# Performance work log

Hardware: AMD Instinct MI355X
Metric: run time of the kernel (lower is better)

The kernel has to match this reference:

```python
import jax, jax.numpy as jnp
import numpy as np

NUM_CLASSES = 80
ROI_SIZE = 7
SAMPLING = 2          # RoIAlign sampling_ratio
STRIDES = (4, 8, 16, 32)
FINEST_SCALE = 56.0
SCORE_THR = 0.05
IOU_THR = 0.5
MAX_PER_IMG = 100
MEANS = jnp.zeros((4,), jnp.float32)
STDS = jnp.array([0.1, 0.1, 0.2, 0.2], jnp.float32)
MAX_RATIO = abs(float(np.log(16.0 / 1000.0)))


def setup_inputs() -> dict:
    key = jax.random.key(0)
    ks = jax.random.split(key, 20)
    C, H0, W0 = 256, 200, 336
    inp = {}
    for i in range(4):
        inp[f"feat{i}"] = jax.random.normal(ks[i], (1, C, H0 >> i, W0 >> i), jnp.float32)
    N = 1000
    IMG_W, IMG_H = 1344.0, 800.0
    cx = jax.random.uniform(ks[4], (N,), minval=0.0, maxval=IMG_W)
    cy = jax.random.uniform(ks[5], (N,), minval=0.0, maxval=IMG_H)
    w = jax.random.uniform(ks[6], (N,), minval=16.0, maxval=512.0)
    h = jax.random.uniform(ks[7], (N,), minval=16.0, maxval=512.0)
    x1 = jnp.clip(cx - w / 2, 0.0, IMG_W - 1)
    y1 = jnp.clip(cy - h / 2, 0.0, IMG_H - 1)
    x2 = jnp.clip(cx + w / 2, x1 + 1.0, IMG_W)
    y2 = jnp.clip(cy + h / 2, y1 + 1.0, IMG_H)
    inp["proposals"] = jnp.stack([x1, y1, x2, y2], axis=-1)
    D = C * ROI_SIZE * ROI_SIZE  # 12544
    FC = 1024
    inp["fc1_w"] = 0.01 * jax.random.normal(ks[8], (FC, D), jnp.float32)
    inp["fc1_b"] = jnp.zeros((FC,), jnp.float32)
    inp["fc2_w"] = 0.01 * jax.random.normal(ks[9], (FC, FC), jnp.float32)
    inp["fc2_b"] = jnp.zeros((FC,), jnp.float32)
    inp["cls_w"] = 0.01 * jax.random.normal(ks[10], (NUM_CLASSES + 1, FC), jnp.float32)
    inp["cls_b"] = jnp.zeros((NUM_CLASSES + 1,), jnp.float32)
    inp["reg_w"] = 0.01 * jax.random.normal(ks[11], (NUM_CLASSES * 4, FC), jnp.float32)
    inp["reg_b"] = jnp.zeros((NUM_CLASSES * 4,), jnp.float32)
    return inp


def _roi_align(feat, rois, scale):
    # feat [C,H,W]; rois [N,4]; aligned RoIAlign, 7x7 out, sampling_ratio=2
    C, H, W = feat.shape
    P = ROI_SIZE * SAMPLING  # 14 uniform sample points per axis

    def one(roi):
        x1, y1, x2, y2 = roi[0], roi[1], roi[2], roi[3]
        sx = x1 * scale - 0.5
        sy = y1 * scale - 0.5
        rw = (x2 - x1) * scale
        rh = (y2 - y1) * scale
        pts = (jnp.arange(P, dtype=feat.dtype) + 0.5) / P
        xs = sx + pts * rw
        ys = sy + pts * rh
        y0 = jnp.floor(ys)
        x0 = jnp.floor(xs)
        ly = ys - y0
        lx = xs - x0
        y0i = jnp.clip(y0.astype(jnp.int32), 0, H - 1)
        y1i = jnp.clip(y0i + 1, 0, H - 1)
        x0i = jnp.clip(x0.astype(jnp.int32), 0, W - 1)
        x1i = jnp.clip(x0i + 1, 0, W - 1)
        g = lambda yi, xi: feat[:, yi[:, None], xi[None, :]]  # [C,P,P]
        ly_ = ly[None, :, None]
        lx_ = lx[None, None, :]
        val = (1 - ly_) * ((1 - lx_) * g(y0i, x0i) + lx_ * g(y0i, x1i)) \
            + ly_ * ((1 - lx_) * g(y1i, x0i) + lx_ * g(y1i, x1i))
        vy = ((ys >= -1.0) & (ys <= H))[None, :, None]
        vx = ((xs >= -1.0) & (xs <= W))[None, None, :]
        val = jnp.where(vy & vx, val, 0.0)
        # average-pool the 2x2 samples per bin -> [C,7,7]
        return val.reshape(C, ROI_SIZE, SAMPLING, ROI_SIZE, SAMPLING).mean(axis=(2, 4))

    return jax.vmap(one)(rois)  # [N,C,7,7]


def _delta2bbox(proposals, deltas):
    d = deltas.reshape(-1, NUM_CLASSES, 4) * STDS + MEANS
    dx, dy = d[..., 0], d[..., 1]
    dw = jnp.clip(d[..., 2], -MAX_RATIO, MAX_RATIO)
    dh = jnp.clip(d[..., 3], -MAX_RATIO, MAX_RATIO)
    px = ((proposals[:, 0] + proposals[:, 2]) * 0.5)[:, None]
    py = ((proposals[:, 1] + proposals[:, 3]) * 0.5)[:, None]
    pw = (proposals[:, 2] - proposals[:, 0])[:, None]
    ph = (proposals[:, 3] - proposals[:, 1])[:, None]
    gw = pw * jnp.exp(dw)
    gh = ph * jnp.exp(dh)
    gx = px + pw * dx
    gy = py + ph * dy
    return jnp.stack([gx - gw * 0.5, gy - gh * 0.5, gx + gw * 0.5, gy + gh * 0.5], axis=-1)


def _pairwise_iou(b):
    x1, y1, x2, y2 = b[:, 0], b[:, 1], b[:, 2], b[:, 3]
    area = jnp.maximum(x2 - x1, 0.0) * jnp.maximum(y2 - y1, 0.0)
    iw = jnp.maximum(jnp.minimum(x2[:, None], x2[None, :]) - jnp.maximum(x1[:, None], x1[None, :]), 0.0)
    ih = jnp.maximum(jnp.minimum(y2[:, None], y2[None, :]) - jnp.maximum(y1[:, None], y1[None, :]), 0.0)
    inter = iw * ih
    return inter / jnp.maximum(area[:, None] + area[None, :] - inter, 1e-8)


def _nms_one_class(boxes, scores):
    # greedy NMS, static shapes; returns score-sorted boxes/scores + keep mask
    N = scores.shape[0]
    order = jnp.argsort(-scores)
    b = boxes[order]
    s = scores[order]
    iou = _pairwise_iou(b)
    idx = jnp.arange(N)

    def body(i, keep):
        sup = (iou[i] > IOU_THR) & keep[i] & (idx > i)
        return keep & jnp.logical_not(sup)

    keep = jax.lax.fori_loop(0, N, body, s > SCORE_THR)
    return b, s, keep


def _batched_nms(bboxes, scores):
    # bboxes [N,81,4], scores [N,81]; class 80 is background (skipped)
    cls_boxes = jnp.transpose(bboxes[:, :NUM_CLASSES, :], (1, 0, 2))  # [80,N,4]
    cls_scores = scores[:, :NUM_CLASSES].T                            # [80,N]
    b, s, keep = jax.vmap(_nms_one_class)(cls_boxes, cls_scores)
    N = s.shape[1]
    s_flat = jnp.where(keep, s, -1.0).reshape(-1)
    topv, topi = jax.lax.top_k(s_flat, MAX_PER_IMG)
    det_boxes = b.reshape(-1, 4)[topi]
    det_classes = (topi // N).astype(jnp.int32)
    valid = topv > 0.0
    num_det = valid.sum().astype(jnp.int32)
    det_scores = jnp.where(valid, topv, 0.0)
    det_boxes = jnp.where(valid[:, None], det_boxes, 0.0)
    det_classes = jnp.where(valid, det_classes, -1)
    return num_det, det_boxes[None], det_scores[None], det_classes[None]


def _forward(feat0, feat1, feat2, feat3, proposals,
             fc1_w, fc1_b, fc2_w, fc2_b, cls_w, cls_b, reg_w, reg_b):
    feats = [feat0[0], feat1[0], feat2[0], feat3[0]]
    wp = proposals[:, 2] - proposals[:, 0]
    hp = proposals[:, 3] - proposals[:, 1]
    scale = jnp.sqrt(jnp.maximum(wp * hp, 1e-6))
    lvl = jnp.clip(jnp.floor(jnp.log2(scale / FINEST_SCALE + 1e-6)), 0, 3).astype(jnp.int32)
    N = proposals.shape[0]
    C = feats[0].shape[0]
    roi_feats = jnp.zeros((N, C, ROI_SIZE, ROI_SIZE), proposals.dtype)
    for l, stride in enumerate(STRIDES):
        f = _roi_align(feats[l], proposals, 1.0 / stride)
        roi_feats = jnp.where((lvl == l)[:, None, None, None], f, roi_feats)
    h = roi_feats.reshape(N, -1)
    h = jax.nn.relu(h @ fc1_w.T + fc1_b)
    h = jax.nn.relu(h @ fc2_w.T + fc2_b)
    cls_score = h @ cls_w.T + cls_b          # [N,81]
    bbox_pred = h @ reg_w.T + reg_b          # [N,320]
    scores = jax.nn.softmax(cls_score, axis=1)
    boxes = _delta2bbox(proposals, bbox_pred)                          # [N,80,4]
    boxes = jnp.concatenate([boxes, jnp.zeros((N, 1, 4), boxes.dtype)], axis=1)
    return _batched_nms(boxes, scores)


def reference(feat0, feat1, feat2, feat3, proposals,
              fc1_w, fc1_b, fc2_w, fc2_b, cls_w, cls_b, reg_w, reg_b):
    return _forward(feat0, feat1, feat2, feat3, proposals,
                    fc1_w, fc1_b, fc2_w, fc2_b, cls_w, cls_b, reg_w, reg_b)
```

## Files before the change

### kernel.cpp

```cpp
#include <hip/hip_runtime.h>
#include <math.h>

#define NCLS   80
#define NPROP  1000
#define FCDIM  1024
#define DFLAT  12544
#define MPAD   1024
#define MAXR   4.1351665567423560f
#define LDSP   40
#define NMSW   16

#define CSPLIT 8
#define CG     (256 / CSPLIT)

typedef unsigned short ushort_t;
typedef unsigned long long ull_t;
using short8  = __attribute__((ext_vector_type(8))) short;
using float4v = __attribute__((ext_vector_type(4))) float;

__device__ inline ushort_t f2bf(float f) {
    unsigned int u = __float_as_uint(f);
    unsigned int r = (u + 0x7fffu + ((u >> 16) & 1u)) >> 16;
    return (ushort_t)r;
}

__global__ __launch_bounds__(256) void roi_align_k(
    const float* __restrict__ f0, const float* __restrict__ f1,
    const float* __restrict__ f2, const float* __restrict__ f3,
    const float* __restrict__ props, ushort_t* __restrict__ Abf)
{
    int r  = blockIdx.x;
    int cz = blockIdx.y;
    int t  = threadIdx.x;

    if (r >= NPROP) {
        for (int i = t; i < CG * 49; i += 256)
            Abf[(size_t)r * DFLAT + cz * (CG * 49) + i] = 0;
        return;
    }

    const float4 p = *(const float4*)&props[(size_t)r * 4];
    float wp = p.z - p.x, hp = p.w - p.y;
    float scale = sqrtf(fmaxf(wp * hp, 1e-6f));
    int lvl = (int)floorf(log2f(scale / 56.0f + 1e-6f));
    lvl = min(max(lvl, 0), 3);

    const float* f; int H, W; float sc;
    switch (lvl) {
        case 0:  f = f0; H = 200; W = 336; sc = 0.25f;    break;
        case 1:  f = f1; H = 100; W = 168; sc = 0.125f;   break;
        case 2:  f = f2; H = 50;  W = 84;  sc = 0.0625f;  break;
        default: f = f3; H = 25;  W = 42;  sc = 0.03125f; break;
    }

    if (t >= 196) return;

    int b   = t >> 2;
    int sub = t & 3;
    int by = b / 7, bx = b - by * 7;
    int sy = by * 2 + (sub >> 1);
    int sx = bx * 2 + (sub & 1);

    float startx = p.x * sc - 0.5f, rangex = (p.z - p.x) * sc;
    float starty = p.y * sc - 0.5f, rangey = (p.w - p.y) * sc;
    float posx = startx + (((float)sx + 0.5f) / 14.0f) * rangex;
    float posy = starty + (((float)sy + 0.5f) / 14.0f) * rangey;

    float flx = floorf(posx), fly = floorf(posy);
    float lx = posx - flx, ly = posy - fly;
    int x0 = min(max((int)flx, 0), W - 1);
    int x1 = min(x0 + 1, W - 1);
    int y0 = min(max((int)fly, 0), H - 1);
    int y1 = min(y0 + 1, H - 1);
    bool valid = (posx >= -1.0f) && (posx <= (float)W) &&
                 (posy >= -1.0f) && (posy <= (float)H);
    float vm = valid ? 0.25f : 0.0f;

    float w00 = (1.f - ly) * (1.f - lx) * vm;
    float w01 = (1.f - ly) * lx * vm;
    float w10 = ly * (1.f - lx) * vm;
    float w11 = ly * lx * vm;
    int o00 = y0 * W + x0, o01 = y0 * W + x1;
    int o10 = y1 * W + x0, o11 = y1 * W + x1;

    const int HW = H * W;
    ushort_t* orow = Abf + (size_t)r * DFLAT + cz * (CG * 49);
    const float* pl = f + (size_t)(cz * CG) * HW;

    #pragma unroll 4
    for (int c = 0; c < CG; c++) {
        float v = pl[o00] * w00 + pl[o01] * w01 + pl[o10] * w10 + pl[o11] * w11;
        v += __shfl_xor(v, 1);
        v += __shfl_xor(v, 2);
        if (sub == 0)
            orow[c * 49 + b] = f2bf(v);
        pl += HW;
    }
}

__global__ __launch_bounds__(256) void gemm_sk_k(
    const ushort_t* __restrict__ A, const float* __restrict__ Wf,
    float* __restrict__ P, int N, int K, int KC)
{
    __shared__ ushort_t As[128 * LDSP];
    __shared__ ushort_t Bs[128 * LDSP];

    int tid = threadIdx.x;
    int w = tid >> 6, l = tid & 63;
    int wm = (w >> 1) * 64, wn = (w & 1) * 64;
    int m0 = blockIdx.y * 128, n0 = blockIdx.x * 128;
    int kc0 = blockIdx.z * KC;

    int lrow = tid >> 2;
    int lko  = (tid & 3) * 8;

    const ushort_t* Ag = A  + (size_t)(m0 + lrow) * K + kc0 + lko;
    const float*    Wg = Wf + (size_t)(n0 + lrow) * K + kc0 + lko;
    size_t rowK64 = (size_t)64 * K;

    float4v acc[4][4];
    #pragma unroll
    for (int i = 0; i < 4; i++)
        #pragma unroll
        for (int j = 0; j < 4; j++)
            acc[i][j] = (float4v){0.f, 0.f, 0.f, 0.f};

    int rl = l & 15, q = l >> 4;

    for (int k0 = 0; k0 < KC; k0 += 32) {
        uint4  a0  = *(const uint4*)(Ag + k0);
        uint4  a1  = *(const uint4*)(Ag + rowK64 + k0);
        float4 w0a = *(const float4*)(Wg + k0);
        float4 w0b = *(const float4*)(Wg + k0 + 4);
        float4 w1a = *(const float4*)(Wg + rowK64 + k0);
        float4 w1b = *(const float4*)(Wg + rowK64 + k0 + 4);

        uint4 wv0, wv1;
        wv0.x = (unsigned)f2bf(w0a.x) | ((unsigned)f2bf(w0a.y) << 16);
        wv0.y = (unsigned)f2bf(w0a.z) | ((unsigned)f2bf(w0a.w) << 16);
        wv0.z = (unsigned)f2bf(w0b.x) | ((unsigned)f2bf(w0b.y) << 16);
        wv0.w = (unsigned)f2bf(w0b.z) | ((unsigned)f2bf(w0b.w) << 16);
        wv1.x = (unsigned)f2bf(w1a.x) | ((unsigned)f2bf(w1a.y) << 16);
        wv1.y = (unsigned)f2bf(w1a.z) | ((unsigned)f2bf(w1a.w) << 16);
        wv1.z = (unsigned)f2bf(w1b.x) | ((unsigned)f2bf(w1b.y) << 16);
        wv1.w = (unsigned)f2bf(w1b.z) | ((unsigned)f2bf(w1b.w) << 16);

        *(uint4*)&As[lrow * LDSP + lko]        = a0;
        *(uint4*)&As[(lrow + 64) * LDSP + lko] = a1;
        *(uint4*)&Bs[lrow * LDSP + lko]        = wv0;
        *(uint4*)&Bs[(lrow + 64) * LDSP + lko] = wv1;
        __syncthreads();

        short8 af[4], bfr[4];
        #pragma unroll
        for (int i = 0; i < 4; i++)
            af[i] = *(const short8*)&As[(wm + i * 16 + rl) * LDSP + q * 8];
        #pragma unroll
        for (int j = 0; j < 4; j++)
            bfr[j] = *(const short8*)&Bs[(wn + j * 16 + rl) * LDSP + q * 8];

        #pragma unroll
        for (int i = 0; i < 4; i++)
            #pragma unroll
            for (int j = 0; j < 4; j++)
                acc[i][j] = __builtin_amdgcn_mfma_f32_16x16x32_bf16(
                    af[i], bfr[j], acc[i][j], 0, 0, 0);
        __syncthreads();
    }

    float* Pz = P + (size_t)blockIdx.z * ((size_t)MPAD * N);
    #pragma unroll
    for (int i = 0; i < 4; i++) {
        #pragma unroll
        for (int j = 0; j < 4; j++) {
            int col = n0 + wn + j * 16 + rl;
            #pragma unroll
            for (int rr = 0; rr < 4; rr++) {
                int row = m0 + wm + i * 16 + q * 4 + rr;
                Pz[(size_t)row * N + col] = acc[i][j][rr];
            }
        }
    }
}

__global__ __launch_bounds__(256) void reduce_sk_k(
    const float* __restrict__ P, const float* __restrict__ bias,
    void* __restrict__ Cout, int N, int SK, int relu, int out_bf16)
{
    size_t idx = ((size_t)blockIdx.x * 256 + threadIdx.x) * 4;
    float4 s = *(const float4*)&P[idx];
    for (int z = 1; z < SK; z++) {
        float4 pv = *(const float4*)&P[(size_t)z * ((size_t)MPAD * N) + idx];
        s.x += pv.x; s.y += pv.y; s.z += pv.z; s.w += pv.w;
    }
    int n = (int)(idx % N);
    float4 b = *(const float4*)&bias[n];
    s.x += b.x; s.y += b.y; s.z += b.z; s.w += b.w;
    if (relu) {
        s.x = fmaxf(s.x, 0.f); s.y = fmaxf(s.y, 0.f);
        s.z = fmaxf(s.z, 0.f); s.w = fmaxf(s.w, 0.f);
    }
    if (out_bf16) {
        ushort4 o;
        o.x = f2bf(s.x); o.y = f2bf(s.y); o.z = f2bf(s.z); o.w = f2bf(s.w);
        *(ushort4*)&((ushort_t*)Cout)[idx] = o;
    } else {
        *(float4*)&((float*)Cout)[idx] = s;
    }
}

__global__ __launch_bounds__(256) void gemm_tn_k(
    const float* __restrict__ A, const float* __restrict__ W,
    const float* __restrict__ bias, float* __restrict__ C,
    int M, int N, int K, int relu)
{
    __shared__ float As[16][64];
    __shared__ float Bs[16][64];

    int tid = threadIdx.x;
    int tx = tid & 15;
    int ty = tid >> 4;
    int m0 = blockIdx.y * 64, n0 = blockIdx.x * 64;

    int lr = tid >> 2;
    int lk = (tid & 3) << 2;

    const float* Arow = A + (size_t)(m0 + lr) * K + lk;
    const float* Wrow = W + (size_t)(n0 + lr) * K + lk;
    bool mOK = (m0 + lr) < M;
    bool nOK = (n0 + lr) < N;

    float acc[4][4] = {};

    for (int k0 = 0; k0 < K; k0 += 16) {
        float4 av = mOK ? *(const float4*)(Arow + k0) : make_float4(0.f, 0.f, 0.f, 0.f);
        float4 wv = nOK ? *(const float4*)(Wrow + k0) : make_float4(0.f, 0.f, 0.f, 0.f);
        As[lk + 0][lr] = av.x; As[lk + 1][lr] = av.y;
        As[lk + 2][lr] = av.z; As[lk + 3][lr] = av.w;
        Bs[lk + 0][lr] = wv.x; Bs[lk + 1][lr] = wv.y;
        Bs[lk + 2][lr] = wv.z; Bs[lk + 3][lr] = wv.w;
        __syncthreads();

        #pragma unroll
        for (int kk = 0; kk < 16; kk++) {
            float4 a = *(const float4*)&As[kk][ty << 2];
            float4 b = *(const float4*)&Bs[kk][tx << 2];
            acc[0][0] += a.x * b.x; acc[0][1] += a.x * b.y;
            acc[0][2] += a.x * b.z; acc[0][3] += a.x * b.w;
            acc[1][0] += a.y * b.x; acc[1][1] += a.y * b.y;
            acc[1][2] += a.y * b.z; acc[1][3] += a.y * b.w;
            acc[2][0] += a.z * b.x; acc[2][1] += a.z * b.y;
            acc[2][2] += a.z * b.z; acc[2][3] += a.z * b.w;
            acc[3][0] += a.w * b.x; acc[3][1] += a.w * b.y;
            acc[3][2] += a.w * b.z; acc[3][3] += a.w * b.w;
        }
        __syncthreads();
    }

    #pragma unroll
    for (int i = 0; i < 4; i++) {
        int m = m0 + (ty << 2) + i;
        if (m >= M) continue;
        #pragma unroll
        for (int j = 0; j < 4; j++) {
            int n = n0 + (tx << 2) + j;
            if (n < N) {
                float v = acc[i][j] + bias[n];
                if (relu) v = fmaxf(v, 0.f);
                C[(size_t)m * N + n] = v;
            }
        }
    }
}

__global__ __launch_bounds__(128) void head_post_k(
    const float* __restrict__ cls_s, const float* __restrict__ reg_s,
    const float* __restrict__ props,
    float* __restrict__ probsT, float* __restrict__ boxesT)
{
    int r = blockIdx.x, t = threadIdx.x;
    __shared__ float red[128];

    float x = (t < 81) ? cls_s[(size_t)r * 81 + t] : -1e30f;
    red[t] = x; __syncthreads();
    for (int s = 64; s > 0; s >>= 1) {
        if (t < s) red[t] = fmaxf(red[t], red[t + s]);
        __syncthreads();
    }
    float mx = red[0];
    __syncthreads();

    float e = (t < 81) ? expf(x - mx) : 0.f;
    red[t] = e; __syncthreads();
    for (int s = 64; s > 0; s >>= 1) {
        if (t < s) red[t] += red[t + s];
        __syncthreads();
    }
    float inv = 1.f / red[0];

    if (t < NCLS) {
        probsT[(size_t)t * NPROP + r] = e * inv;

        const float4 p = *(const float4*)&props[(size_t)r * 4];
        float4 d = *(const float4*)&reg_s[(size_t)r * 320 + t * 4];
        float dx = d.x * 0.1f, dy = d.y * 0.1f;
        float dw = fminf(fmaxf(d.z * 0.2f, -MAXR), MAXR);
        float dh = fminf(fmaxf(d.w * 0.2f, -MAXR), MAXR);
        float px = (p.x + p.z) * 0.5f, py = (p.y + p.w) * 0.5f;
        float pw = p.z - p.x, ph = p.w - p.y;
        float gw = pw * expf(dw), gh = ph * expf(dh);
        float gx = px + pw * dx, gy = py + ph * dy;
        float4 bo = make_float4(gx - gw * 0.5f, gy - gh * 0.5f,
                                gx + gw * 0.5f, gy + gh * 0.5f);
        *(float4*)&boxesT[(size_t)(t * NPROP + r) * 4] = bo;
    }
}

__global__ __launch_bounds__(512) void sort_k(
    const float* __restrict__ probsT, const float* __restrict__ boxesT,
    float* __restrict__ sortedS, float* __restrict__ sortedB)
{
    int c = blockIdx.x, t = threadIdx.x;
    __shared__ float sk[1024];
    __shared__ int   si[1024];

    for (int j = t; j < 1024; j += 512) {
        sk[j] = (j < NPROP) ? probsT[(size_t)c * NPROP + j] : -1e30f;
        si[j] = j;
    }
    __syncthreads();

    for (int size = 2; size <= 1024; size <<= 1) {
        for (int stride = size >> 1; stride > 0; stride >>= 1) {
            int i = (t << 1) - (t & (stride - 1));
            int j = i + stride;
            float ka = sk[i], kb = sk[j];
            int ia = si[i], ib = si[j];
            bool aFirst = (ka > kb) || (ka == kb && ia < ib);
            bool desc = ((i & size) == 0);
            if (desc ? !aFirst : aFirst) {
                sk[i] = kb; sk[j] = ka; si[i] = ib; si[j] = ia;
            }
            __syncthreads();
        }
    }

    for (int j = t; j < NPROP; j += 512) {
        sortedS[(size_t)c * NPROP + j] = sk[j];
        const float4 bb = *(const float4*)&boxesT[(size_t)(c * NPROP + si[j]) * 4];
        *(float4*)&sortedB[(size_t)(c * NPROP + j) * 4] = bb;
    }
}

__global__ __launch_bounds__(256) void nms_mask_k(
    const float* __restrict__ sortedS, const float* __restrict__ sortedB,
    ull_t* __restrict__ masks)
{
    int c = blockIdx.x;
    int i = blockIdx.y * 256 + threadIdx.x;
    __shared__ float x1s[NPROP], y1s[NPROP], x2s[NPROP], y2s[NPROP], ars[NPROP];

    for (int j = threadIdx.x; j < NPROP; j += 256) {
        float4 b = *(const float4*)&sortedB[(size_t)(c * NPROP + j) * 4];
        x1s[j] = b.x; y1s[j] = b.y; x2s[j] = b.z; y2s[j] = b.w;
        ars[j] = fmaxf(b.z - b.x, 0.f) * fmaxf(b.w - b.y, 0.f);
    }
    __syncthreads();

    if (i >= NPROP) return;
    if (!(sortedS[(size_t)c * NPROP + i] > 0.05f)) return;

    float xi1 = x1s[i], yi1 = y1s[i], xi2 = x2s[i], yi2 = y2s[i], ai = ars[i];
    ull_t* row = masks + ((size_t)c * NPROP + i) * NMSW;

    for (int w = 0; w < NMSW; w++) {
        ull_t m = 0ull;
        int j0 = w << 6;
        #pragma unroll 4
        for (int k = 0; k < 64; k++) {
            int j = j0 + k;
            if (j < NPROP) {
                float iw = fmaxf(fminf(xi2, x2s[j]) - fmaxf(xi1, x1s[j]), 0.f);
                float ih = fmaxf(fminf(yi2, y2s[j]) - fmaxf(yi1, y1s[j]), 0.f);
                float inter = iw * ih;
                float iou = inter / fmaxf(ai + ars[j] - inter, 1e-8f);
                if (iou > 0.5f) m |= (1ull << k);
            }
        }
        row[w] = m;
    }
}

__global__ __launch_bounds__(256) void nms_scan_k(
    const float* __restrict__ sortedS, const ull_t* __restrict__ masks,
    float* __restrict__ candS, int* __restrict__ candI)
{
    int c = blockIdx.x, t = threadIdx.x;
    __shared__ unsigned char kp[NPROP];
    __shared__ int segc[256];

    for (int j = t; j < NPROP; j += 256)
        kp[j] = sortedS[(size_t)c * NPROP + j] > 0.05f ? 1 : 0;
    __syncthreads();

    if (t < 64) {
        const ull_t* M = masks + (size_t)c * NPROP * NMSW;
        ull_t rem = 0ull;
        for (int i = 0; i < NPROP; i++) {
            if (kp[i]) {
                ull_t w = __shfl(rem, i >> 6);
                if ((w >> (i & 63)) & 1ull) {
                    if (t == 0) kp[i] = 0;
                } else {
                    if (t < NMSW) rem |= M[(size_t)i * NMSW + t];
                }
            }
        }
    }
    __syncthreads();

    int j0 = t * 4;
    int cnt = 0;
    #pragma unroll
    for (int k = 0; k < 4; k++) {
        int j = j0 + k;
        if (j < NPROP && kp[j]) cnt++;
    }
    segc[t] = cnt;
    __syncthreads();
    for (int off = 1; off < 256; off <<= 1) {
        int add = (t >= off) ? segc[t - off] : 0;
        __syncthreads();
        segc[t] += add;
        __syncthreads();
    }
    int pos = segc[t] - cnt;
    #pragma unroll
    for (int k = 0; k < 4; k++) {
        int j = j0 + k;
        if (j < NPROP && kp[j]) {
            if (pos < 100) {
                candS[c * 100 + pos] = sortedS[(size_t)c * NPROP + j];
                candI[c * 100 + pos] = c * NPROP + j;
            }
            pos++;
        }
    }
    int total = segc[255];
    for (int p = total + t; p < 100; p += 256) {
        candS[c * 100 + p] = -2e30f;
        candI[c * 100 + p] = 0x7fffffff;
    }
}

__global__ __launch_bounds__(128) void merge_k(
    const float* __restrict__ candS, const int* __restrict__ candI,
    const float* __restrict__ sortedB, float* __restrict__ out)
{
    int t = threadIdx.x;
    __shared__ int   head[NCLS];
    __shared__ float topv[100];
    __shared__ int   topi[100];

    if (t < NCLS) head[t] = 0;
    __syncthreads();

    for (int r = 0; r < 100; r++) {
        if (t < 64) {
            float v = -2e30f; int fi = 0x7fffffff; int cls = 0;
            {
                int h = head[t];
                if (h < 100) { v = candS[t * 100 + h]; fi = candI[t * 100 + h]; cls = t; }
            }
            int c2 = t + 64;
            if (c2 < NCLS) {
                int h = head[c2];
                if (h < 100) {
                    float v2 = candS[c2 * 100 + h]; int fi2 = candI[c2 * 100 + h];
                    if (v2 > v || (v2 == v && fi2 < fi)) { v = v2; fi = fi2; cls = c2; }
                }
            }
            #pragma unroll
            for (int s = 1; s < 64; s <<= 1) {
                float ov = __shfl_xor(v, s);
                int ofi  = __shfl_xor(fi, s);
                int ocl  = __shfl_xor(cls, s);
                if (ov > v || (ov == v && ofi < fi)) { v = ov; fi = ofi; cls = ocl; }
            }
            if (t == 0) { topv[r] = v; topi[r] = fi; head[cls]++; }
        }
        __syncthreads();
    }

    if (t < 100) {
        float v = topv[t]; int fi = topi[t];
        bool valid = v > 0.0f;
        float4 bb = make_float4(0.f, 0.f, 0.f, 0.f);
        if (valid) bb = *(const float4*)&sortedB[(size_t)fi * 4];
        out[1 + t * 4 + 0] = bb.x;
        out[1 + t * 4 + 1] = bb.y;
        out[1 + t * 4 + 2] = bb.z;
        out[1 + t * 4 + 3] = bb.w;
        out[401 + t] = valid ? v : 0.0f;
        out[501 + t] = valid ? (float)(fi / NPROP) : -1.0f;
    }
    if (t == 0) {
        int n = 0;
        for (int r = 0; r < 100; r++) n += (topv[r] > 0.0f) ? 1 : 0;
        out[0] = (float)n;
    }
}

extern "C" void kernel_launch(void* const* d_in, const int* in_sizes, int n_in,
                              void* d_out, int out_size, void* d_ws, size_t ws_size,
                              hipStream_t stream)
{
    const float* f0    = (const float*)d_in[0];
    const float* f1    = (const float*)d_in[1];
    const float* f2    = (const float*)d_in[2];
    const float* f3    = (const float*)d_in[3];
    const float* props = (const float*)d_in[4];
    const float* fc1_w = (const float*)d_in[5];
    const float* fc1_b = (const float*)d_in[6];
    const float* fc2_w = (const float*)d_in[7];
    const float* fc2_b = (const float*)d_in[8];
    const float* cls_w = (const float*)d_in[9];
    const float* cls_b = (const float*)d_in[10];
    const float* reg_w = (const float*)d_in[11];
    const float* reg_b = (const float*)d_in[12];
    float* out = (float*)d_out;

    unsigned char* base = (unsigned char*)d_ws;
    ushort_t* Abf  = (ushort_t*)(base);
    ushort_t* h1   = (ushort_t*)(base + 25690112);
    float*    P1   = (float*)(base + 27787264);
    float*    P2   = (float*)(base + 27787264);
    float*    h2   = (float*)(base + 44564480);
    float*    cls_s   = (float*)(base + 48758784);
    float*    reg_s   = (float*)(base + 49090560);
    float*    probsT  = (float*)(base + 50401280);
    float*    boxesT  = (float*)(base + 50721280);
    float*    sortedS = (float*)(base + 52001280);
    float*    sortedB = (float*)(base + 52321280);
    float*    candS   = (float*)(base + 53601280);
    int*      candI   = (int*)(base + 53633280);
    ull_t*    masks   = (ull_t*)(base);

    roi_align_k<<<dim3(MPAD, CSPLIT), 256, 0, stream>>>(f0, f1, f2, f3, props, Abf);

    gemm_sk_k<<<dim3(FCDIM / 128, MPAD / 128, 8), 256, 0, stream>>>(
        Abf, fc1_w, P1, FCDIM, DFLAT, DFLAT / 8);
    reduce_sk_k<<<(MPAD * FCDIM / 4) / 256, 256, 0, stream>>>(
        P1, fc1_b, h1, FCDIM, 8, 1, 1);

    gemm_sk_k<<<dim3(FCDIM / 128, MPAD / 128, 4), 256, 0, stream>>>(
        h1, fc2_w, P2, FCDIM, FCDIM, FCDIM / 4);
    reduce_sk_k<<<(MPAD * FCDIM / 4) / 256, 256, 0, stream>>>(
        P2, fc2_b, h2, FCDIM, 4, 1, 0);

    gemm_tn_k<<<dim3((81 + 63) / 64, (NPROP + 63) / 64), 256, 0, stream>>>(
        h2, cls_w, cls_b, cls_s, NPROP, 81, FCDIM, 0);
    gemm_tn_k<<<dim3((320 + 63) / 64, (NPROP + 63) / 64), 256, 0, stream>>>(
        h2, reg_w, reg_b, reg_s, NPROP, 320, FCDIM, 0);

    head_post_k<<<NPROP, 128, 0, stream>>>(cls_s, reg_s, props, probsT, boxesT);
    sort_k<<<NCLS, 512, 0, stream>>>(probsT, boxesT, sortedS, sortedB);
    nms_mask_k<<<dim3(NCLS, (NPROP + 255) / 256), 256, 0, stream>>>(
        sortedS, sortedB, masks);
    nms_scan_k<<<NCLS, 256, 0, stream>>>(sortedS, masks, candS, candI);
    merge_k<<<1, 128, 0, stream>>>(candS, candI, sortedB, out);
}
```

Baseline: 676.6 us.

## Vectorize RoIAlign corner loads and merge cls/reg head GEMMs into one

RoIAlign now loads the two horizontal bilinear neighbours as one float2 per row, folding weights when the sample sits on the right edge, so each channel takes two loads instead of four. The cls and reg weight matrices are copied into one padded 404-row matrix by a new kernel, and a single GEMM produces both head outputs, removing one launch. The trade-off is an extra weight copy kernel each call, plus float2 loads that may be only 4-byte aligned when the offset is odd.

```diff
diff --git a/kernel.cpp b/kernel.cpp
--- a/kernel.cpp
+++ b/kernel.cpp
@@ -9,6 +9,7 @@
 #define MAXR   4.1351665567423560f
 #define LDSP   40
 #define NMSW   16
+#define NCAT   404
 
 #define CSPLIT 8
 #define CG     (256 / CSPLIT)
@@ -69,7 +70,6 @@
     float flx = floorf(posx), fly = floorf(posy);
     float lx = posx - flx, ly = posy - fly;
     int x0 = min(max((int)flx, 0), W - 1);
-    int x1 = min(x0 + 1, W - 1);
     int y0 = min(max((int)fly, 0), H - 1);
     int y1 = min(y0 + 1, H - 1);
     bool valid = (posx >= -1.0f) && (posx <= (float)W) &&
@@ -80,8 +80,13 @@
     float w01 = (1.f - ly) * lx * vm;
     float w10 = ly * (1.f - lx) * vm;
     float w11 = ly * lx * vm;
-    int o00 = y0 * W + x0, o01 = y0 * W + x1;
-    int o10 = y1 * W + x0, o11 = y1 * W + x1;
+
+    int  xb = min(x0, W - 2);
+    bool xr = (x0 == W - 1);
+    float wtA = xr ? 0.f : w00, wtB = xr ? (w00 + w01) : w01;
+    float wbA = xr ? 0.f : w10, wbB = xr ? (w10 + w11) : w11;
+    int ot = y0 * W + xb;
+    int ob = y1 * W + xb;
 
     const int HW = H * W;
     ushort_t* orow = Abf + (size_t)r * DFLAT + cz * (CG * 49);
@@ -89,7 +94,9 @@
 
     #pragma unroll 4
     for (int c = 0; c < CG; c++) {
-        float v = pl[o00] * w00 + pl[o01] * w01 + pl[o10] * w10 + pl[o11] * w11;
+        float2 tv = *(const float2*)(pl + ot);
+        float2 bv = *(const float2*)(pl + ob);
+        float v = tv.x * wtA + tv.y * wtB + bv.x * wbA + bv.y * wbB;
         v += __shfl_xor(v, 1);
         v += __shfl_xor(v, 2);
         if (sub == 0)
@@ -207,6 +214,26 @@
     } else {
         *(float4*)&((float*)Cout)[idx] = s;
     }
+}
+
+__global__ __launch_bounds__(256) void concat_w_k(
+    const float* __restrict__ reg_w, const float* __restrict__ cls_w,
+    const float* __restrict__ reg_b, const float* __restrict__ cls_b,
+    float* __restrict__ Wcat, float* __restrict__ bcat)
+{
+    int row = blockIdx.x;
+    int t = threadIdx.x;
+    float4 v = make_float4(0.f, 0.f, 0.f, 0.f);
+    float bv = 0.f;
+    if (row < 320) {
+        v = *(const float4*)&reg_w[(size_t)row * FCDIM + t * 4];
+        bv = reg_b[row];
+    } else if (row < NCAT - 3) {
+        v = *(const float4*)&cls_w[(size_t)(row - 320) * FCDIM + t * 4];
+        bv = cls_b[row - 320];
+    }
+    *(float4*)&Wcat[(size_t)row * FCDIM + t * 4] = v;
+    if (t == 0) bcat[row] = bv;
 }
 
 __global__ __launch_bounds__(256) void gemm_tn_k(
@@ -274,14 +301,13 @@
 }
 
 __global__ __launch_bounds__(128) void head_post_k(
-    const float* __restrict__ cls_s, const float* __restrict__ reg_s,
-    const float* __restrict__ props,
+    const float* __restrict__ hr_s, const float* __restrict__ props,
     float* __restrict__ probsT, float* __restrict__ boxesT)
 {
     int r = blockIdx.x, t = threadIdx.x;
     __shared__ float red[128];
 
-    float x = (t < 81) ? cls_s[(size_t)r * 81 + t] : -1e30f;
+    float x = (t < 81) ? hr_s[(size_t)r * NCAT + 320 + t] : -1e30f;
     red[t] = x; __syncthreads();
     for (int s = 64; s > 0; s >>= 1) {
         if (t < s) red[t] = fmaxf(red[t], red[t + s]);
@@ -302,7 +328,7 @@
         probsT[(size_t)t * NPROP + r] = e * inv;
 
         const float4 p = *(const float4*)&props[(size_t)r * 4];
-        float4 d = *(const float4*)&reg_s[(size_t)r * 320 + t * 4];
+        float4 d = *(const float4*)&hr_s[(size_t)r * NCAT + t * 4];
         float dx = d.x * 0.1f, dy = d.y * 0.1f;
         float dw = fminf(fmaxf(d.z * 0.2f, -MAXR), MAXR);
         float dh = fminf(fmaxf(d.w * 0.2f, -MAXR), MAXR);
@@ -536,14 +562,15 @@
     float*    P1   = (float*)(base + 27787264);
     float*    P2   = (float*)(base + 27787264);
     float*    h2   = (float*)(base + 44564480);
-    float*    cls_s   = (float*)(base + 48758784);
-    float*    reg_s   = (float*)(base + 49090560);
+    float*    hr_s    = (float*)(base + 48758784);
     float*    probsT  = (float*)(base + 50401280);
     float*    boxesT  = (float*)(base + 50721280);
     float*    sortedS = (float*)(base + 52001280);
     float*    sortedB = (float*)(base + 52321280);
     float*    candS   = (float*)(base + 53601280);
     int*      candI   = (int*)(base + 53633280);
+    float*    Wcat    = (float*)(base + 53665280);
+    float*    bcat    = (float*)(base + 55320064);
     ull_t*    masks   = (ull_t*)(base);
 
     roi_align_k<<<dim3(MPAD, CSPLIT), 256, 0, stream>>>(f0, f1, f2, f3, props, Abf);
@@ -553,17 +580,17 @@
     reduce_sk_k<<<(MPAD * FCDIM / 4) / 256, 256, 0, stream>>>(
         P1, fc1_b, h1, FCDIM, 8, 1, 1);
 
+    concat_w_k<<<NCAT, 256, 0, stream>>>(reg_w, cls_w, reg_b, cls_b, Wcat, bcat);
+
     gemm_sk_k<<<dim3(FCDIM / 128, MPAD / 128, 4), 256, 0, stream>>>(
         h1, fc2_w, P2, FCDIM, FCDIM, FCDIM / 4);
     reduce_sk_k<<<(MPAD * FCDIM / 4) / 256, 256, 0, stream>>>(
         P2, fc2_b, h2, FCDIM, 4, 1, 0);
 
-    gemm_tn_k<<<dim3((81 + 63) / 64, (NPROP + 63) / 64), 256, 0, stream>>>(
-        h2, cls_w, cls_b, cls_s, NPROP, 81, FCDIM, 0);
-    gemm_tn_k<<<dim3((320 + 63) / 64, (NPROP + 63) / 64), 256, 0, stream>>>(
-        h2, reg_w, reg_b, reg_s, NPROP, 320, FCDIM, 0);
-
-    head_post_k<<<NPROP, 128, 0, stream>>>(cls_s, reg_s, props, probsT, boxesT);
+    gemm_tn_k<<<dim3((NCAT + 63) / 64, (NPROP + 63) / 64), 256, 0, stream>>>(
+        h2, Wcat, bcat, hr_s, NPROP, NCAT, FCDIM, 0);
+
+    head_post_k<<<NPROP, 128, 0, stream>>>(hr_s, props, probsT, boxesT);
     sort_k<<<NCLS, 512, 0, stream>>>(probsT, boxesT, sortedS, sortedB);
     nms_mask_k<<<dim3(NCLS, (NPROP + 255) / 256), 256, 0, stream>>>(
         sortedS, sortedB, masks);
```

Measured after the change: 577.6 us. 1.17x faster.
